# Optimization experiments

Measured on AMD Instinct MI355X. Metric: run time of the kernel, lower is better.

## Reference

```python
import jax, jax.numpy as jnp
import numpy as np

NX, NY = 4096, 4096
T = 1.0
TIME_STEPS = 400
DT = T / TIME_STEPS
DX = 1.0 / (NX - 1)
DY = 1.0 / (NY - 1)
Z = 1.0
FROG = 2
BC = jnp.array([-1.0, 1.0], dtype=jnp.float32)


def _conv_ax0(A, f):
    # valid cross-correlation along axis 0 (matches F.conv1d after transpose)
    L = f.shape[0]
    n = A.shape[0] - L + 1
    out = f[0] * A[0:n, :]
    for k in range(1, L):
        out = out + f[k] * A[k:k + n, :]
    return out


def _conv_ax1(A, f):
    L = f.shape[0]
    n = A.shape[1] - L + 1
    out = f[0] * A[:, 0:n]
    for k in range(1, L):
        out = out + f[k] * A[:, k:k + n]
    return out


def _amper(E, Hx, Hy, f, s):
    # S1: d/dx of Hy ; S2: d/dy of Hx
    S1 = (Z * DT / DX) * _conv_ax0(Hy, f)[0:-1, s:NY - s]
    S2 = (Z * DT / DY) * _conv_ax1(Hx, f)[s:NX - s, 0:-1]
    return E[s:NX - s, s:NY - s] + S1 - S2


def _faraday(E, Hx, Hy, f, s):
    S3 = (DT / (Z * DY)) * _conv_ax1(E, f)[s:NX - s, :]
    S4 = (DT / (Z * DX)) * _conv_ax0(E, f)[:, s:NY - s]
    Ax = Hx[s:NX - s, s - 1:NY - s] - S3
    Ay = Hy[s - 1:NX - s, s:NY - s] + S4
    return Ax, Ay


def setup_inputs() -> dict:
    key = jax.random.key(0)
    k1, k2, k3 = jax.random.split(key, 3)
    X1 = jax.random.normal(k1, (NX, NY), dtype=jnp.float32)
    X2 = jax.random.normal(k2, (NX, NY), dtype=jnp.float32)
    X3 = jax.random.normal(k3, (NX, NY), dtype=jnp.float32)
    w1 = jnp.ones((1,), dtype=jnp.float32)
    return {"X1": X1, "X2": X2, "X3": X3, "w1": w1}


def reference(X1, X2, X3, w1):
    f4 = jnp.concatenate([(w1 - 1.0) / 3.0, -w1, w1, (1.0 - w1) / 3.0])
    E, Hx, Hy = X1, X2, X3
    # boundary-order then interior (frog) Ampere update of E
    E = E.at[1:NX - 1, 1:NY - 1].set(_amper(X1, X2, X3, BC, 1))
    E = E.at[FROG:NX - FROG, FROG:NY - FROG].set(_amper(E, X2, X3, f4, FROG))
    # Faraday updates of Hx, Hy from the ORIGINAL fields (bc order)
    Ax1, Ay1 = _faraday(X1, X2, X3, BC, 1)
    Hx = Hx.at[1:NX - 1, 0:NY - 1].set(Ax1)
    Hy = Hy.at[0:NX - 1, 1:NY - 1].set(Ay1)
    # interior Faraday updates using updated E, Hx, Hy
    Ax2, Ay2 = _faraday(E, Hx, Hy, f4, FROG)
    Hx = Hx.at[FROG:NX - FROG, FROG - 1:NY - FROG].set(Ax2)
    Hy = Hy.at[FROG - 1:NX - FROG, FROG:NY - FROG].set(Ay2)
    return (E, Hx, Hy)
```

## Files before the change

### kernel.cpp

```cpp
#include <hip/hip_runtime.h>

#define NXg 4096
#define NYg 4096
#define RPT 16
#define ROW0 8
#define NBANDS 255

static constexpr float C = 10.2375f;

struct F7  { float v[7];  };
struct F10 { float v[10]; };

__device__ __forceinline__ void ld12(const float* __restrict__ P, int r, int c0,
                                     float4& a, float4& b, float4& c) {
    const size_t o = (size_t)r * NYg + c0;
    a = *(const float4*)(P + o - 4);
    b = *(const float4*)(P + o);
    c = *(const float4*)(P + o + 4);
}

__device__ __forceinline__ F7 mk7(const float4& a, const float4& b, const float4& c) {
    F7 r;
    r.v[0] = a.w; r.v[1] = b.x; r.v[2] = b.y; r.v[3] = b.z;
    r.v[4] = b.w; r.v[5] = c.x; r.v[6] = c.y;
    return r;
}
__device__ __forceinline__ F10 mk10(const float4& a, const float4& b, const float4& c) {
    F10 r;
    r.v[0] = a.y; r.v[1] = a.z; r.v[2] = a.w;
    r.v[3] = b.x; r.v[4] = b.y; r.v[5] = b.z; r.v[6] = b.w;
    r.v[7] = c.x; r.v[8] = c.y; r.v[9] = c.z;
    return r;
}

__device__ __forceinline__ F7 ld7(const float* __restrict__ P, int r, int c0) {
    float4 a, b, c; ld12(P, r, c0, a, b, c); return mk7(a, b, c);
}
__device__ __forceinline__ F10 ld10(const float* __restrict__ P, int r, int c0) {
    float4 a, b, c; ld12(P, r, c0, a, b, c); return mk10(a, b, c);
}

__global__ __launch_bounds__(256, 3) void fat_kernel(
    const float* __restrict__ X1, const float* __restrict__ X2,
    const float* __restrict__ X3, const float* __restrict__ w1,
    float* __restrict__ E, float* __restrict__ Hx, float* __restrict__ Hy)
{
    const int t  = threadIdx.x;
    const int c0 = (blockIdx.x * 256 + t) * 4;
    const int i0 = ROW0 + blockIdx.y * RPT;
    const bool gL = (c0 == 0);
    const bool gR = (c0 == NYg - 4);

    const float wv = w1[0];
    const float f0 = (wv - 1.0f) / 3.0f;
    const float f1 = -wv;
    const float f2 = wv;
    const float f3 = (1.0f - wv) / 3.0f;

    auto eRow = [&](const F7& x3m2, const F7& x3m1, const F7& x3p0, const F7& x3p1,
                    const F10& x2r, const F7& x1r) -> F7 {
        F7 e;
        #pragma unroll
        for (int m = 0; m < 7; ++m) {
            const float e1 = x1r.v[m] + C * (x3p0.v[m] - x3m1.v[m])
                                      - C * (x2r.v[m + 2] - x2r.v[m + 1]);
            e.v[m] = e1
                + C * (f0 * x3m2.v[m] + f1 * x3m1.v[m] + f2 * x3p0.v[m] + f3 * x3p1.v[m])
                - C * (f0 * x2r.v[m] + f1 * x2r.v[m + 1] + f2 * x2r.v[m + 2] + f3 * x2r.v[m + 3]);
        }
        if (gL) {
            e.v[1] = x1r.v[1];
            e.v[2] = x1r.v[2] + C * (x3p0.v[2] - x3m1.v[2])
                              - C * (x2r.v[4] - x2r.v[3]);
        }
        if (gR) {
            e.v[4] = x1r.v[4];
            e.v[3] = x1r.v[3] + C * (x3p0.v[3] - x3m1.v[3])
                              - C * (x2r.v[5] - x2r.v[4]);
        }
        return e;
    };

    F7 p3a = ld7(X3, i0 - 3, c0);
    F7 p3b = ld7(X3, i0 - 2, c0);
    F7 p3c = ld7(X3, i0 - 1, c0);
    F7 w3[4];
    w3[0] = ld7(X3, i0,     c0);
    w3[1] = ld7(X3, i0 + 1, c0);
    w3[2] = ld7(X3, i0 + 2, c0);
    w3[3] = ld7(X3, i0 + 3, c0);

    F10 q2a = ld10(X2, i0 - 1, c0);
    F10 q2b = ld10(X2, i0,     c0);
    F10 q2c = ld10(X2, i0 + 1, c0);
    F10 w2r = ld10(X2, i0 + 2, c0);

    F7 q1a = ld7(X1, i0 - 1, c0);
    F7 w1r[3];
    w1r[0] = ld7(X1, i0,     c0);
    w1r[1] = ld7(X1, i0 + 1, c0);
    w1r[2] = ld7(X1, i0 + 2, c0);

    F7 ew[4];
    ew[0] = eRow(p3a, p3b, p3c, w3[0], q2a, q1a);
    ew[1] = eRow(p3b, p3c, w3[0], w3[1], q2b, w1r[0]);
    ew[2] = eRow(p3c, w3[0], w3[1], w3[2], q2c, w1r[1]);

    float x2c0[4] = {q2b.v[3], q2b.v[4], q2b.v[5], q2b.v[6]};
    float x2c1[4] = {q2c.v[3], q2c.v[4], q2c.v[5], q2c.v[6]};

    #pragma unroll
    for (int s = 0; s < RPT; ++s) {
        const int i = i0 + s;

        F7  t3; F10 t2; F7 t1;
        if (s < RPT - 1) {
            t3 = ld7(X3, i + 4, c0);
            t2 = ld10(X2, i + 3, c0);
            t1 = ld7(X1, i + 3, c0);
        }

        ew[3] = eRow(w3[0], w3[1], w3[2], w3[3], w2r, w1r[2]);

        float hx[4], hy[4];
        #pragma unroll
        for (int q = 0; q < 4; ++q) {
            hx[q] = x2c0[q] - C * (w1r[0].v[q + 2] - w1r[0].v[q + 1])
                  - C * (f0 * ew[1].v[q]     + f1 * ew[1].v[q + 1]
                       + f2 * ew[1].v[q + 2] + f3 * ew[1].v[q + 3]);
            hy[q] = w3[0].v[q + 1] + C * (w1r[1].v[q + 1] - w1r[0].v[q + 1])
                  + C * (f0 * ew[0].v[q + 1] + f1 * ew[1].v[q + 1]
                       + f2 * ew[2].v[q + 1] + f3 * ew[3].v[q + 1]);
        }
        if (gL) {
            hx[0] = x2c0[0] - C * (w1r[0].v[2] - w1r[0].v[1]);
            hy[0] = w3[0].v[1];
            hy[1] = w3[0].v[2] + C * (w1r[1].v[2] - w1r[0].v[2]);
        }
        if (gR) {
            hx[3] = x2c0[3];
            hy[3] = w3[0].v[4];
            hx[2] = x2c0[2] - C * (w1r[0].v[4] - w1r[0].v[3]);
            hy[2] = w3[0].v[3] + C * (w1r[1].v[3] - w1r[0].v[3]);
        }

        const size_t idx = (size_t)i * NYg + c0;
        *(float4*)(E  + idx) = make_float4(ew[1].v[1], ew[1].v[2], ew[1].v[3], ew[1].v[4]);
        *(float4*)(Hx + idx) = make_float4(hx[0], hx[1], hx[2], hx[3]);
        *(float4*)(Hy + idx) = make_float4(hy[0], hy[1], hy[2], hy[3]);

        ew[0] = ew[1]; ew[1] = ew[2]; ew[2] = ew[3];
        w3[0] = w3[1]; w3[1] = w3[2]; w3[2] = w3[3];
        w1r[0] = w1r[1]; w1r[1] = w1r[2];
        #pragma unroll
        for (int q = 0; q < 4; ++q) { x2c0[q] = x2c1[q]; x2c1[q] = w2r.v[3 + q]; }
        if (s < RPT - 1) { w3[3] = t3; w2r = t2; w1r[2] = t1; }
    }
}

#define TRE 8
#define EROWSE 12
#define ECOLSE 136

__global__ __launch_bounds__(256) void edge_kernel(
    const float* __restrict__ X1, const float* __restrict__ X2,
    const float* __restrict__ X3, const float* __restrict__ w1,
    float* __restrict__ E, float* __restrict__ Hx, float* __restrict__ Hy)
{
    __shared__ float elds[EROWSE][ECOLSE];
    const int t    = threadIdx.x;
    const int row0 = blockIdx.y ? (NXg - TRE) : 0;
    const int col0 = blockIdx.x * 128;

    const float wv = w1[0];
    const float f0 = (wv - 1.0f) / 3.0f;
    const float f1 = -wv;
    const float f2 = wv;
    const float f3 = (1.0f - wv) / 3.0f;

    for (int cidx = t; cidx < EROWSE * ECOLSE; cidx += 256) {
        const int r  = cidx / ECOLSE;
        const int cc = cidx - r * ECOLSE;
        const int gr = row0 - 2 + r;
        const int gc = col0 - 4 + cc;
        float e = 0.0f;
        if (gr >= 0 && gr < NXg && gc >= 0 && gc < NYg) {
            const size_t idx = (size_t)gr * NYg + gc;
            const float x1 = X1[idx];
            if (gr == 0 || gr == NXg - 1 || gc == 0 || gc == NYg - 1) {
                e = x1;
            } else {
                float e1 = x1 + C * (X3[idx] - X3[idx - NYg])
                              - C * (X2[idx] - X2[idx - 1]);
                if (gr >= 2 && gr <= NXg - 3 && gc >= 2 && gc <= NYg - 3) {
                    e1 += C * (f0 * X3[idx - 2 * NYg] + f1 * X3[idx - NYg]
                             + f2 * X3[idx] + f3 * X3[idx + NYg])
                        - C * (f0 * X2[idx - 2] + f1 * X2[idx - 1]
                             + f2 * X2[idx] + f3 * X2[idx + 1]);
                }
                e = e1;
            }
        }
        elds[r][cc] = e;
    }
    __syncthreads();

    for (int cidx = t; cidx < TRE * 128; cidx += 256) {
        const int hr  = cidx >> 7;
        const int tc  = cidx & 127;
        const int gr  = row0 + hr;
        const int gcc = col0 + tc;
        const size_t idx = (size_t)gr * NYg + gcc;
        const int lr  = hr + 2;
        const int lc2 = tc + 4;

        const float ec = elds[lr][lc2];
        E[idx] = ec;

        const float x1 = X1[idx];

        float hx = X2[idx];
        if (gr >= 1 && gr <= NXg - 2 && gcc <= NYg - 2)
            hx -= C * (X1[idx + 1] - x1);
        if (gr >= 2 && gr <= NXg - 3 && gcc >= 1 && gcc <= NYg - 3) {
            hx -= C * (f0 * elds[lr][lc2 - 1] + f1 * ec
                     + f2 * elds[lr][lc2 + 1] + f3 * elds[lr][lc2 + 2]);
        }
        Hx[idx] = hx;

        float hy = X3[idx];
        if (gr <= NXg - 2 && gcc >= 1 && gcc <= NYg - 2)
            hy += C * (X1[idx + NYg] - x1);
        if (gr >= 1 && gr <= NXg - 3 && gcc >= 2 && gcc <= NYg - 3) {
            hy += C * (f0 * elds[lr - 1][lc2] + f1 * ec
                     + f2 * elds[lr + 1][lc2] + f3 * elds[lr + 2][lc2]);
        }
        Hy[idx] = hy;
    }
}

extern "C" void kernel_launch(void* const* d_in, const int* in_sizes, int n_in,
                              void* d_out, int out_size, void* d_ws, size_t ws_size,
                              hipStream_t stream) {
    const float* X1 = (const float*)d_in[0];
    const float* X2 = (const float*)d_in[1];
    const float* X3 = (const float*)d_in[2];
    const float* w1 = (const float*)d_in[3];

    float* E  = (float*)d_out;
    float* Hx = (float*)d_out + (size_t)NXg * NYg;
    float* Hy = (float*)d_out + 2 * (size_t)NXg * NYg;

    edge_kernel<<<dim3(32, 2),     256, 0, stream>>>(X1, X2, X3, w1, E, Hx, Hy);
    fat_kernel <<<dim3(4, NBANDS), 256, 0, stream>>>(X1, X2, X3, w1, E, Hx, Hy);
}
```

Baseline: 115.8 us.

## Replace register-streaming row bands with one-row-per-block stencil kernel

Drops the 16-row register-rotating band loop in favour of a kernel where each block computes a single output row, loading all needed neighbour rows and recomputing the three extra E rows locally. This exposes many more blocks and removes the serial dependency chain and high register pressure. In exchange each output row re-reads about 15 input row segments and recomputes E for neighbouring rows, which raises global/L2 traffic and arithmetic. The kernel launch order is also swapped so the edge kernel runs after the main kernel.

```diff
diff --git a/kernel.cpp b/kernel.cpp
--- a/kernel.cpp
+++ b/kernel.cpp
@@ -2,12 +2,12 @@
 
 #define NXg 4096
 #define NYg 4096
-#define RPT 16
 #define ROW0 8
-#define NBANDS 255
+#define NROWS 4080
 
 static constexpr float C = 10.2375f;
 
+struct F4  { float v[4];  };
 struct F7  { float v[7];  };
 struct F10 { float v[10]; };
 
@@ -18,36 +18,39 @@
     b = *(const float4*)(P + o);
     c = *(const float4*)(P + o + 4);
 }
-
-__device__ __forceinline__ F7 mk7(const float4& a, const float4& b, const float4& c) {
-    F7 r;
-    r.v[0] = a.w; r.v[1] = b.x; r.v[2] = b.y; r.v[3] = b.z;
-    r.v[4] = b.w; r.v[5] = c.x; r.v[6] = c.y;
-    return r;
-}
-__device__ __forceinline__ F10 mk10(const float4& a, const float4& b, const float4& c) {
-    F10 r;
-    r.v[0] = a.y; r.v[1] = a.z; r.v[2] = a.w;
-    r.v[3] = b.x; r.v[4] = b.y; r.v[5] = b.z; r.v[6] = b.w;
-    r.v[7] = c.x; r.v[8] = c.y; r.v[9] = c.z;
-    return r;
-}
-
 __device__ __forceinline__ F7 ld7(const float* __restrict__ P, int r, int c0) {
-    float4 a, b, c; ld12(P, r, c0, a, b, c); return mk7(a, b, c);
+    float4 a, b, c; ld12(P, r, c0, a, b, c);
+    F7 x;
+    x.v[0] = a.w; x.v[1] = b.x; x.v[2] = b.y; x.v[3] = b.z;
+    x.v[4] = b.w; x.v[5] = c.x; x.v[6] = c.y;
+    return x;
 }
 __device__ __forceinline__ F10 ld10(const float* __restrict__ P, int r, int c0) {
-    float4 a, b, c; ld12(P, r, c0, a, b, c); return mk10(a, b, c);
-}
-
-__global__ __launch_bounds__(256, 3) void fat_kernel(
+    float4 a, b, c; ld12(P, r, c0, a, b, c);
+    F10 x;
+    x.v[0] = a.y; x.v[1] = a.z; x.v[2] = a.w;
+    x.v[3] = b.x; x.v[4] = b.y; x.v[5] = b.z; x.v[6] = b.w;
+    x.v[7] = c.x; x.v[8] = c.y; x.v[9] = c.z;
+    return x;
+}
+__device__ __forceinline__ F4 ldb(const float* __restrict__ P, int r, int c0) {
+    const float4 b = *(const float4*)(P + (size_t)r * NYg + c0);
+    F4 x; x.v[0] = b.x; x.v[1] = b.y; x.v[2] = b.z; x.v[3] = b.w;
+    return x;
+}
+__device__ __forceinline__ F4 mid(const F7& s) {
+    F4 x; x.v[0] = s.v[1]; x.v[1] = s.v[2]; x.v[2] = s.v[3]; x.v[3] = s.v[4];
+    return x;
+}
+
+__global__ __launch_bounds__(256) void row_kernel(
     const float* __restrict__ X1, const float* __restrict__ X2,
     const float* __restrict__ X3, const float* __restrict__ w1,
     float* __restrict__ E, float* __restrict__ Hx, float* __restrict__ Hy)
 {
     const int t  = threadIdx.x;
     const int c0 = (blockIdx.x * 256 + t) * 4;
-    const int i0 = ROW0 + blockIdx.y * RPT;
+    const int i  = ROW0 + blockIdx.y;
     const bool gL = (c0 == 0);
     const bool gR = (c0 == NYg - 4);
 
@@ -57,105 +60,99 @@
     const float f2 = wv;
     const float f3 = (1.0f - wv) / 3.0f;
 
-    auto eRow = [&](const F7& x3m2, const F7& x3m1, const F7& x3p0, const F7& x3p1,
-                    const F10& x2r, const F7& x1r) -> F7 {
-        F7 e;
+    const F4  x3m3 = ldb(X3, i - 3, c0);
+    const F7  x3m2 = ld7(X3, i - 2, c0);
+    const F7  x3m1 = ld7(X3, i - 1, c0);
+    const F7  x3i  = ld7(X3, i,     c0);
+    const F7  x3p1 = ld7(X3, i + 1, c0);
+    const F4  x3p2 = ldb(X3, i + 2, c0);
+    const F4  x3p3 = ldb(X3, i + 3, c0);
+
+    const F10 x2m1 = ld10(X2, i - 1, c0);
+    const F10 x2i  = ld10(X2, i,     c0);
+    const F10 x2p1 = ld10(X2, i + 1, c0);
+    const F10 x2p2 = ld10(X2, i + 2, c0);
+
+    const F4  x1m1 = ldb(X1, i - 1, c0);
+    const F7  x1i  = ld7(X1, i,     c0);
+    const F4  x1p1 = ldb(X1, i + 1, c0);
+    const F4  x1p2 = ldb(X1, i + 2, c0);
+
+    F7 e7;
+    #pragma unroll
+    for (int m = 0; m < 7; ++m) {
+        const float e1 = x1i.v[m] + C * (x3i.v[m] - x3m1.v[m])
+                                  - C * (x2i.v[m + 2] - x2i.v[m + 1]);
+        e7.v[m] = e1
+            + C * (f0 * x3m2.v[m] + f1 * x3m1.v[m] + f2 * x3i.v[m] + f3 * x3p1.v[m])
+            - C * (f0 * x2i.v[m] + f1 * x2i.v[m + 1] + f2 * x2i.v[m + 2] + f3 * x2i.v[m + 3]);
+    }
+    if (gL) {
+        e7.v[1] = x1i.v[1];
+        e7.v[2] = x1i.v[2] + C * (x3i.v[2] - x3m1.v[2])
+                           - C * (x2i.v[4] - x2i.v[3]);
+    }
+    if (gR) {
+        e7.v[4] = x1i.v[4];
+        e7.v[3] = x1i.v[3] + C * (x3i.v[3] - x3m1.v[3])
+                           - C * (x2i.v[5] - x2i.v[4]);
+    }
+
+    auto eRow4 = [&](const F4& a, const F4& b, const F4& cc, const F4& d,
+                     const F10& x2r, const F4& x1r) -> F4 {
+        F4 e;
         #pragma unroll
-        for (int m = 0; m < 7; ++m) {
-            const float e1 = x1r.v[m] + C * (x3p0.v[m] - x3m1.v[m])
-                                      - C * (x2r.v[m + 2] - x2r.v[m + 1]);
-            e.v[m] = e1
-                + C * (f0 * x3m2.v[m] + f1 * x3m1.v[m] + f2 * x3p0.v[m] + f3 * x3p1.v[m])
-                - C * (f0 * x2r.v[m] + f1 * x2r.v[m + 1] + f2 * x2r.v[m + 2] + f3 * x2r.v[m + 3]);
+        for (int q = 0; q < 4; ++q) {
+            const float e1 = x1r.v[q] + C * (cc.v[q] - b.v[q])
+                                      - C * (x2r.v[q + 3] - x2r.v[q + 2]);
+            e.v[q] = e1
+                + C * (f0 * a.v[q] + f1 * b.v[q] + f2 * cc.v[q] + f3 * d.v[q])
+                - C * (f0 * x2r.v[q + 1] + f1 * x2r.v[q + 2]
+                     + f2 * x2r.v[q + 3] + f3 * x2r.v[q + 4]);
         }
         if (gL) {
-            e.v[1] = x1r.v[1];
-            e.v[2] = x1r.v[2] + C * (x3p0.v[2] - x3m1.v[2])
+            e.v[0] = x1r.v[0];
+            e.v[1] = x1r.v[1] + C * (cc.v[1] - b.v[1])
                               - C * (x2r.v[4] - x2r.v[3]);
         }
         if (gR) {
-            e.v[4] = x1r.v[4];
-            e.v[3] = x1r.v[3] + C * (x3p0.v[3] - x3m1.v[3])
+            e.v[3] = x1r.v[3];
+            e.v[2] = x1r.v[2] + C * (cc.v[2] - b.v[2])
                               - C * (x2r.v[5] - x2r.v[4]);
         }
         return e;
     };
 
-    F7 p3a = ld7(X3, i0 - 3, c0);
-    F7 p3b = ld7(X3, i0 - 2, c0);
-    F7 p3c = ld7(X3, i0 - 1, c0);
-    F7 w3[4];
-    w3[0] = ld7(X3, i0,     c0);
-    w3[1] = ld7(X3, i0 + 1, c0);
-    w3[2] = ld7(X3, i0 + 2, c0);
-    w3[3] = ld7(X3, i0 + 3, c0);
-
-    F10 q2a = ld10(X2, i0 - 1, c0);
-    F10 q2b = ld10(X2, i0,     c0);
-    F10 q2c = ld10(X2, i0 + 1, c0);
-    F10 w2r = ld10(X2, i0 + 2, c0);
-
-    F7 q1a = ld7(X1, i0 - 1, c0);
-    F7 w1r[3];
-    w1r[0] = ld7(X1, i0,     c0);
-    w1r[1] = ld7(X1, i0 + 1, c0);
-    w1r[2] = ld7(X1, i0 + 2, c0);
-
-    F7 ew[4];
-    ew[0] = eRow(p3a, p3b, p3c, w3[0], q2a, q1a);
-    ew[1] = eRow(p3b, p3c, w3[0], w3[1], q2b, w1r[0]);
-    ew[2] = eRow(p3c, w3[0], w3[1], w3[2], q2c, w1r[1]);
-
-    float x2c0[4] = {q2b.v[3], q2b.v[4], q2b.v[5], q2b.v[6]};
-    float x2c1[4] = {q2c.v[3], q2c.v[4], q2c.v[5], q2c.v[6]};
-
+    const F4 em1 = eRow4(x3m3,      mid(x3m2), mid(x3m1), mid(x3i), x2m1, x1m1);
+    const F4 ep1 = eRow4(mid(x3m1), mid(x3i),  mid(x3p1), x3p2,     x2p1, x1p1);
+    const F4 ep2 = eRow4(mid(x3i),  mid(x3p1), x3p2,      x3p3,     x2p2, x1p2);
+
+    float hx[4], hy[4];
     #pragma unroll
-    for (int s = 0; s < RPT; ++s) {
-        const int i = i0 + s;
-
-        F7  t3; F10 t2; F7 t1;
-        if (s < RPT - 1) {
-            t3 = ld7(X3, i + 4, c0);
-            t2 = ld10(X2, i + 3, c0);
-            t1 = ld7(X1, i + 3, c0);
-        }
-
-        ew[3] = eRow(w3[0], w3[1], w3[2], w3[3], w2r, w1r[2]);
-
-        float hx[4], hy[4];
-        #pragma unroll
-        for (int q = 0; q < 4; ++q) {
-            hx[q] = x2c0[q] - C * (w1r[0].v[q + 2] - w1r[0].v[q + 1])
-                  - C * (f0 * ew[1].v[q]     + f1 * ew[1].v[q + 1]
-                       + f2 * ew[1].v[q + 2] + f3 * ew[1].v[q + 3]);
-            hy[q] = w3[0].v[q + 1] + C * (w1r[1].v[q + 1] - w1r[0].v[q + 1])
-                  + C * (f0 * ew[0].v[q + 1] + f1 * ew[1].v[q + 1]
-                       + f2 * ew[2].v[q + 1] + f3 * ew[3].v[q + 1]);
-        }
-        if (gL) {
-            hx[0] = x2c0[0] - C * (w1r[0].v[2] - w1r[0].v[1]);
-            hy[0] = w3[0].v[1];
-            hy[1] = w3[0].v[2] + C * (w1r[1].v[2] - w1r[0].v[2]);
-        }
-        if (gR) {
-            hx[3] = x2c0[3];
-            hy[3] = w3[0].v[4];
-            hx[2] = x2c0[2] - C * (w1r[0].v[4] - w1r[0].v[3]);
-            hy[2] = w3[0].v[3] + C * (w1r[1].v[3] - w1r[0].v[3]);
-        }
-
-        const size_t idx = (size_t)i * NYg + c0;
-        *(float4*)(E  + idx) = make_float4(ew[1].v[1], ew[1].v[2], ew[1].v[3], ew[1].v[4]);
-        *(float4*)(Hx + idx) = make_float4(hx[0], hx[1], hx[2], hx[3]);
-        *(float4*)(Hy + idx) = make_float4(hy[0], hy[1], hy[2], hy[3]);
-
-        ew[0] = ew[1]; ew[1] = ew[2]; ew[2] = ew[3];
-        w3[0] = w3[1]; w3[1] = w3[2]; w3[2] = w3[3];
-        w1r[0] = w1r[1]; w1r[1] = w1r[2];
-        #pragma unroll
-        for (int q = 0; q < 4; ++q) { x2c0[q] = x2c1[q]; x2c1[q] = w2r.v[3 + q]; }
-        if (s < RPT - 1) { w3[3] = t3; w2r = t2; w1r[2] = t1; }
-    }
+    for (int q = 0; q < 4; ++q) {
+        hx[q] = x2i.v[q + 3] - C * (x1i.v[q + 2] - x1i.v[q + 1])
+              - C * (f0 * e7.v[q] + f1 * e7.v[q + 1]
+                   + f2 * e7.v[q + 2] + f3 * e7.v[q + 3]);
+        hy[q] = x3i.v[q + 1] + C * (x1p1.v[q] - x1i.v[q + 1])
+              + C * (f0 * em1.v[q] + f1 * e7.v[q + 1]
+                   + f2 * ep1.v[q] + f3 * ep2.v[q]);
+    }
+    if (gL) {
+        hx[0] = x2i.v[3] - C * (x1i.v[2] - x1i.v[1]);
+        hy[0] = x3i.v[1];
+        hy[1] = x3i.v[2] + C * (x1p1.v[1] - x1i.v[2]);
+    }
+    if (gR) {
+        hx[3] = x2i.v[6];
+        hy[3] = x3i.v[4];
+        hx[2] = x2i.v[5] - C * (x1i.v[4] - x1i.v[3]);
+        hy[2] = x3i.v[3] + C * (x1p1.v[2] - x1i.v[3]);
+    }
+
+    const size_t idx = (size_t)i * NYg + c0;
+    *(float4*)(E  + idx) = make_float4(e7.v[1], e7.v[2], e7.v[3], e7.v[4]);
+    *(float4*)(Hx + idx) = make_float4(hx[0], hx[1], hx[2], hx[3]);
+    *(float4*)(Hy + idx) = make_float4(hy[0], hy[1], hy[2], hy[3]);
 }
 
 #define TRE 8
@@ -251,6 +248,6 @@
     float* Hx = (float*)d_out + (size_t)NXg * NYg;
     float* Hy = (float*)d_out + 2 * (size_t)NXg * NYg;
 
-    edge_kernel<<<dim3(32, 2),     256, 0, stream>>>(X1, X2, X3, w1, E, Hx, Hy);
-    fat_kernel <<<dim3(4, NBANDS), 256, 0, stream>>>(X1, X2, X3, w1, E, Hx, Hy);
-}
+    row_kernel <<<dim3(NYg / 1024, NROWS), 256, 0, stream>>>(X1, X2, X3, w1, E, Hx, Hy);
+    edge_kernel<<<dim3(32, 2), 256, 0, stream>>>(X1, X2, X3, w1, E, Hx, Hy);
+}
```

After: 135.9 us. +17.4%, slower.
